# Performance work log

Hardware: AMD Instinct MI355X
Metric: run time of the kernel (lower is better)

Reference implementation:

```python
import jax, jax.numpy as jnp
import numpy as np

B, T, DIN, DOUT, H = 16, 4096, 64, 64, 128


def setup_inputs() -> dict:
    key = jax.random.key(0)
    ks = jax.random.split(key, 8)
    s_in = 1.0 / np.sqrt(DIN)       # ~ torch kaiming-uniform scale for Linear
    s_h = 0.5 / np.sqrt(2.0 * H)    # keep complex recurrence spectral radius ~0.5
    s_out = 1.0 / np.sqrt(H)
    return {
        "x_real": jax.random.normal(ks[0], (B, T, DIN), jnp.float32),
        "x_imag": jax.random.normal(ks[1], (B, T, DIN), jnp.float32),
        "Wi_real": jax.random.normal(ks[2], (H, DIN), jnp.float32) * s_in,
        "Wi_imag": jax.random.normal(ks[3], (H, DIN), jnp.float32) * s_in,
        "Wh_real": jax.random.normal(ks[4], (H, H), jnp.float32) * s_h,
        "Wh_imag": jax.random.normal(ks[5], (H, H), jnp.float32) * s_h,
        "Wo_real": jax.random.normal(ks[6], (DOUT, H), jnp.float32) * s_out,
        "Wo_imag": jax.random.normal(ks[7], (DOUT, H), jnp.float32) * s_out,
    }


def reference(x_real, x_imag, Wi_real, Wi_imag, Wh_real, Wh_imag, Wo_real, Wo_imag):
    # Recombine real/imag parts into complex64 (torch module uses complex Linear layers).
    x = x_real + 1j * x_imag                       # [B, T, DIN] complex64
    Wi = Wi_real + 1j * Wi_imag                    # [H, DIN]
    Wh = Wh_real + 1j * Wh_imag                    # [H, H]
    Wo = Wo_real + 1j * Wo_imag                    # [DOUT, H]

    # input_ff: torch Linear computes x @ W^T
    xp = jnp.einsum("btd,hd->bth", x, Wi)          # [B, T, H]

    WhT = Wh.T

    def step(h, xt):
        # h_{t+1} = x_proj_t + 1j * hidden_ff(h_t)
        h_next = xt + 1j * (h @ WhT)
        return h_next, h_next

    h0 = jnp.zeros((x.shape[0], Wh.shape[0]), dtype=xp.dtype)   # [B, H]
    _, hs = jax.lax.scan(step, h0, jnp.swapaxes(xp, 0, 1))      # hs: [T, B, H]
    hidden = jnp.swapaxes(hs, 0, 1)                             # [B, T, H]

    # output_ff
    out = jnp.einsum("bth,oh->bto", hidden, Wo)                 # [B, T, DOUT] complex64
    return out
```

## Files before the change

kernel.cpp:

```cpp
#include <hip/hip_runtime.h>
#include <stdint.h>

#define BB   16
#define TT   4096
#define DIN  64
#define DOUT 64
#define HH   128
#define LCH  64
#define WARM 32
#define SS   96
#define TAPS 32


typedef __attribute__((ext_vector_type(8))) short short8;
typedef __attribute__((ext_vector_type(4))) float f32x4;

__device__ __forceinline__ uint32_t f2bf(float f) {
  uint32_t x = __float_as_uint(f);
  return (x + 0x7FFFu + ((x >> 16) & 1u)) >> 16;
}
__device__ __forceinline__ uint32_t pack_bf(float re, float im) {
  return f2bf(re) | (f2bf(im) << 16);
}
__device__ __forceinline__ float bf_re(uint32_t u) { return __uint_as_float(u << 16); }
__device__ __forceinline__ float bf_im(uint32_t u) { return __uint_as_float(u & 0xFFFF0000u); }

__device__ __forceinline__ int fragIdx(int d, int o, int part, int kk) {
  const int ks = part * 2 + (kk >> 5);
  const int k32 = kk & 31;
  const int nt = o >> 4;
  const int lane = ((k32 >> 3) << 4) | (o & 15);
  return (((d * 16 + ks * 4 + nt) * 64) + lane) * 8 + (k32 & 7);
}

__device__ __forceinline__ void rot_i(int r, float re, float im,
                                      float& tr, float& ti) {
  switch (r & 3) {
    case 0: tr = re;  ti = im;  break;
    case 1: tr = -im; ti = re;  break;
    case 2: tr = -re; ti = -im; break;
    default: tr = im; ti = -re; break;
  }
}

__device__ __forceinline__ void matsq_dev(
    const float* __restrict__ ar, const float* __restrict__ ai,
    int fromPlanes, const float2* __restrict__ src, float2* __restrict__ dst,
    int tileId, unsigned char* smemraw) {
  float2* band  = (float2*)smemraw;
  float2* panel = (float2*)(smemraw + 16384);
  const int tid = threadIdx.x;
  const int ib = tileId >> 3, jb = tileId & 7;
  for (int idx = tid; idx < 16 * HH; idx += 512) {
    const int e = (ib * 16 + (idx >> 7)) * HH + (idx & 127);
    band[idx] = fromPlanes ? make_float2(ar[e], ai[e]) : src[e];
  }
  const int jt = tid & 15, it = (tid >> 4) & 15;
  float sre = 0.f, sim = 0.f;
  for (int kp = 0; kp < 4; ++kp) {
    __syncthreads();
    for (int idx = tid; idx < 32 * HH; idx += 512) {
      const int e = (kp * 32 + (idx >> 7)) * HH + (idx & 127);
      panel[idx] = fromPlanes ? make_float2(ar[e], ai[e]) : src[e];
    }
    __syncthreads();
    if (tid < 256) {
#pragma unroll 4
      for (int kk = 0; kk < 32; ++kk) {
        const float2 a = band[it * HH + kp * 32 + kk];
        const float2 bv = panel[kk * HH + jb * 16 + jt];
        sre = fmaf(a.x, bv.x, sre); sre = fmaf(-a.y, bv.y, sre);
        sim = fmaf(a.x, bv.y, sim); sim = fmaf(a.y, bv.x, sim);
      }
    }
  }
  if (tid < 256)
    dst[(ib * 16 + it) * HH + jb * 16 + jt] = make_float2(sre, sim);
}

__device__ __forceinline__ void pmul_dev(
    const float* __restrict__ ar, const float* __restrict__ ai, int aPlanes,
    const float2* __restrict__ Aflat,
    const float* __restrict__ sr, const float* __restrict__ si, int sPlanes,
    const float2* __restrict__ src,
    float2* __restrict__ dst, int tile, unsigned char* smemraw) {
  float2* Pl = (float2*)smemraw;
  const int tid = threadIdx.x;
  if (sPlanes) {
    for (int idx = tid; idx < 8192; idx += 512)
      Pl[idx] = make_float2(sr[idx], si[idx]);
  } else {
    const float4* s4 = (const float4*)src;
    float4* d4 = (float4*)Pl;
    for (int idx = tid; idx < 4096; idx += 512) d4[idx] = s4[idx];
  }
  __syncthreads();
  if (tid < 256) {
    const int i = tile * 16 + (tid >> 4);
    const int c0 = (tid & 15) * 4;
    float accr[4] = {0.f, 0.f, 0.f, 0.f}, acim[4] = {0.f, 0.f, 0.f, 0.f};
#pragma unroll 4
    for (int k = 0; k < 128; ++k) {
      const float2 a = aPlanes ? make_float2(ar[i * 128 + k], ai[i * 128 + k])
                               : Aflat[i * 128 + k];
      const float4 p01 = *(const float4*)&Pl[k * 64 + c0];
      const float4 p23 = *(const float4*)&Pl[k * 64 + c0 + 2];
      accr[0] = fmaf(a.x, p01.x, fmaf(-a.y, p01.y, accr[0]));
      acim[0] = fmaf(a.x, p01.y, fmaf(a.y, p01.x, acim[0]));
      accr[1] = fmaf(a.x, p01.z, fmaf(-a.y, p01.w, accr[1]));
      acim[1] = fmaf(a.x, p01.w, fmaf(a.y, p01.z, acim[1]));
      accr[2] = fmaf(a.x, p23.x, fmaf(-a.y, p23.y, accr[2]));
      acim[2] = fmaf(a.x, p23.y, fmaf(a.y, p23.x, acim[2]));
      accr[3] = fmaf(a.x, p23.z, fmaf(-a.y, p23.w, accr[3]));
      acim[3] = fmaf(a.x, p23.w, fmaf(a.y, p23.z, acim[3]));
    }
#pragma unroll
    for (int cc = 0; cc < 4; ++cc)
      dst[i * 64 + c0 + cc] = make_float2(accr[cc], acim[cc]);
  }
}

__global__ __launch_bounds__(512, 1) void k_s0(
    const float* __restrict__ wir, const float* __restrict__ wii,
    const float* __restrict__ whr, const float* __restrict__ whi,
    float2* __restrict__ ws) {
  __shared__ __align__(16) unsigned char smem[65536];
  float2* Wp0 = ws;
  float2* P   = ws + 32768;
  const int blk = blockIdx.x;
  if (blk < 64) {
    matsq_dev(whr, whi, 1, Wp0, Wp0, blk, smem);
  } else if (blk < 72) {
    pmul_dev(whr, whi, 1, Wp0, wir, wii, 1, Wp0, P + 8192, blk - 64, smem);
  } else {
    const int idx = (blk - 72) * 512 + threadIdx.x;
    P[idx] = make_float2(wir[idx], wii[idx]);
  }
}

__global__ __launch_bounds__(512, 1) void k_s1(
    const float* __restrict__ wir, const float* __restrict__ wii,
    float2* __restrict__ ws) {
  __shared__ __align__(16) unsigned char smem[65536];
  float2* Wp0 = ws;
  float2* Wp1 = ws + 16384;
  float2* P   = ws + 32768;
  const int blk = blockIdx.x;
  if (blk < 64) {
    matsq_dev(nullptr, nullptr, 0, Wp0, Wp1, blk, smem);
  } else if (blk < 72) {
    pmul_dev(nullptr, nullptr, 0, Wp0, wir, wii, 0, P,
             P + 16384, blk - 64, smem);
  } else {
    pmul_dev(nullptr, nullptr, 0, Wp0, wir, wii, 0, P + 8192,
             P + 24576, blk - 72, smem);
  }
}

__global__ __launch_bounds__(512, 1) void k_chain4(
    const float* __restrict__ wor, const float* __restrict__ woi,
    float2* __restrict__ ws) {
  __shared__ __align__(16) unsigned char smemraw[73472];
  const float2* P  = ws + 32768;
  const float2* M4 = ws + 16384;
  short* Wf = (short*)(ws + 65536);
  const int kk = (int)blockIdx.x >> 1;
  const int u  = (int)blockIdx.x & 1;
  float2* pb = (float2*)smemraw;
  float2* wo = (float2*)(smemraw + 4352);
  const int tid = threadIdx.x;
  const int mi = tid >> 2, mq = tid & 3;
  const int vo = tid >> 3, vg = tid & 7;

  float m4re[32], m4im[32];
  {
    const float4* g = (const float4*)(M4 + mi * 128 + mq * 32);
#pragma unroll
    for (int s = 0; s < 16; ++s) {
      const float4 v = g[s];
      m4re[2 * s] = v.x; m4im[2 * s] = v.y;
      m4re[2 * s + 1] = v.z; m4im[2 * s + 1] = v.w;
    }
  }
  for (int idx = tid; idx < 8192; idx += 512) {
    const int o = idx >> 7, h = idx & 127;
    wo[o * 135 + h + (h >> 4)] = make_float2(wor[o * 128 + h], woi[o * 128 + h]);
  }
  if (tid < 128) {
    pb[tid + (tid >> 4)]       = P[(size_t)u * 8192 + tid * 64 + kk];
    pb[272 + tid + (tid >> 4)] = P[(size_t)(u + 2) * 8192 + tid * 64 + kk];
  }
  __syncthreads();

  int cur = 0;
#pragma unroll 1
  for (int j = 0; j < 8; ++j) {
    const float2* qa = pb + cur * 136;
    const float2* qb = pb + 272 + cur * 136;
    float var = 0.f, vai = 0.f, vbr = 0.f, vbi = 0.f;
    {
      const float2* wrow = wo + vo * 135 + vg * 17;
      const float2* pra = qa + vg * 17;
      const float2* prb = qb + vg * 17;
#pragma unroll
      for (int s = 0; s < 16; ++s) {
        const float2 a = wrow[s];
        const float2 pa = pra[s];
        const float2 pv = prb[s];
        var = fmaf(a.x, pa.x, fmaf(-a.y, pa.y, var));
        vai = fmaf(a.x, pa.y, fmaf(a.y, pa.x, vai));
        vbr = fmaf(a.x, pv.x, fmaf(-a.y, pv.y, vbr));
        vbi = fmaf(a.x, pv.y, fmaf(a.y, pv.x, vbi));
      }
    }
    var += __shfl_xor(var, 1); vai += __shfl_xor(vai, 1);
    vbr += __shfl_xor(vbr, 1); vbi += __shfl_xor(vbi, 1);
    var += __shfl_xor(var, 2); vai += __shfl_xor(vai, 2);
    vbr += __shfl_xor(vbr, 2); vbi += __shfl_xor(vbi, 2);
    var += __shfl_xor(var, 4); vai += __shfl_xor(vai, 4);
    vbr += __shfl_xor(vbr, 4); vbi += __shfl_xor(vbi, 4);
    if (vg == 0) {
      float tr, ti;
      rot_i(u, var, vai, tr, ti);
      const int da = 4 * j + u;
      Wf[fragIdx(da, vo, 0, kk)] = (short)f2bf(tr);
      Wf[fragIdx(da, vo, 1, kk)] = (short)f2bf(-ti);
      rot_i(u + 2, vbr, vbi, tr, ti);
      const int db = 4 * j + u + 2;
      Wf[fragIdx(db, vo, 0, kk)] = (short)f2bf(tr);
      Wf[fragIdx(db, vo, 1, kk)] = (short)f2bf(-ti);
    }
    if (j < 7) {
      float nar = 0.f, nai = 0.f, nbr = 0.f, nbi = 0.f;
      const float2* pma = qa + mq * 34;
      const float2* pmb = qb + mq * 34;
#pragma unroll
      for (int s = 0; s < 32; ++s) {
        const float2 pa = pma[s + (s >> 4)];
        const float2 pv = pmb[s + (s >> 4)];
        nar = fmaf(m4re[s], pa.x, fmaf(-m4im[s], pa.y, nar));
        nai = fmaf(m4re[s], pa.y, fmaf(m4im[s], pa.x, nai));
        nbr = fmaf(m4re[s], pv.x, fmaf(-m4im[s], pv.y, nbr));
        nbi = fmaf(m4re[s], pv.y, fmaf(m4im[s], pv.x, nbi));
      }
      nar += __shfl_xor(nar, 1); nai += __shfl_xor(nai, 1);
      nbr += __shfl_xor(nbr, 1); nbi += __shfl_xor(nbi, 1);
      nar += __shfl_xor(nar, 2); nai += __shfl_xor(nai, 2);
      nbr += __shfl_xor(nbr, 2); nbi += __shfl_xor(nbi, 2);
      if (mq == 0) {
        pb[(cur ^ 1) * 136 + mi + (mi >> 4)] = make_float2(nar, nai);
        pb[272 + (cur ^ 1) * 136 + mi + (mi >> 4)] = make_float2(nbr, nbi);
      }
    }
    __syncthreads();
    cur ^= 1;
  }
}

__global__ __launch_bounds__(512, 1) void k_conv2(
    const float* __restrict__ xr, const float* __restrict__ xi,
    const short* __restrict__ Wf, float* __restrict__ out) {
  __shared__ __align__(16) unsigned char smem[73728];
  char* xs = (char*)smem;
  const int tid = threadIdx.x;
  const int b = blockIdx.x & 15;
  const int t0 = (blockIdx.x >> 4) * 256;

  for (int idx = tid; idx < 288 * 16; idx += 512) {
    const int r = idx >> 4;
    const int kq = (idx & 15) << 2;
    const int sw = (r & 7) << 4;
    const int t = t0 + r - 32;
    uint32_t r01 = 0u, r23 = 0u, i01 = 0u, i23 = 0u;
    if (t >= 0) {
      const size_t g = ((size_t)b * TT + t) * 64 + kq;
      const float4 vr = *(const float4*)(xr + g);
      const float4 vi = *(const float4*)(xi + g);
      r01 = f2bf(vr.x) | (f2bf(vr.y) << 16);
      r23 = f2bf(vr.z) | (f2bf(vr.w) << 16);
      i01 = f2bf(vi.x) | (f2bf(vi.y) << 16);
      i23 = f2bf(vi.z) | (f2bf(vi.w) << 16);
    }
    char* rowp = xs + r * 256;
    *(uint2*)(rowp + ((kq * 2) ^ sw))       = make_uint2(r01, r23);
    *(uint2*)(rowp + ((128 + kq * 2) ^ sw)) = make_uint2(i01, i23);
  }
  __syncthreads();

  const int w = tid >> 6;
  const int lane = tid & 63;
  const int wr = w >> 1;
  const int kh = w & 1;
  const int lm = lane & 15;
  const int kc8 = (lane >> 4) << 3;

  f32x4 acc[4][4];
#pragma unroll
  for (int mi = 0; mi < 4; ++mi)
#pragma unroll
    for (int nt = 0; nt < 4; ++nt) acc[mi][nt] = (f32x4){0.f, 0.f, 0.f, 0.f};

  short8 aqA[4], bqA[4], aqB[4], bqB[4];
#define FETCH(IT, AQ, BQ)                                                     \
  do {                                                                        \
    const int d_ = kh * 16 + ((IT) >> 2);                                     \
    const int ks_ = (IT) & 3;                                                 \
    const int rb_ = 32 - d_ + wr * 64 + lm;                                   \
    const int colb_ = ((ks_ >> 1) * 64 + (ks_ & 1) * 32 + kc8) * 2;           \
    _Pragma("unroll")                                                         \
    for (int nt_ = 0; nt_ < 4; ++nt_)                                         \
      BQ[nt_] = *(const short8*)(Wf +                                         \
          (((d_ * 16 + ks_ * 4 + nt_) * 64 + lane) << 3));                    \
    _Pragma("unroll")                                                         \
    for (int mi_ = 0; mi_ < 4; ++mi_) {                                       \
      const int r_ = rb_ + mi_ * 16;                                          \
      AQ[mi_] = *(const short8*)(xs + r_ * 256 +                              \
                                 (colb_ ^ ((r_ & 7) << 4)));                  \
    }                                                                         \
  } while (0)

#define MFMAGRP(AQ, BQ)                                                       \
  do {                                                                        \
    _Pragma("unroll")                                                         \
    for (int mi_ = 0; mi_ < 4; ++mi_)                                         \
      _Pragma("unroll")                                                       \
      for (int nt_ = 0; nt_ < 4; ++nt_)                                       \
        acc[mi_][nt_] = __builtin_amdgcn_mfma_f32_16x16x32_bf16(              \
            AQ[mi_], BQ[nt_], acc[mi_][nt_], 0, 0, 0);                        \
  } while (0)

  FETCH(0, aqA, bqA);
#pragma unroll 1
  for (int it = 0; it < 62; it += 2) {
    FETCH(it + 1, aqB, bqB);
    MFMAGRP(aqA, bqA);
    FETCH(it + 2, aqA, bqA);
    MFMAGRP(aqB, bqB);
  }
  FETCH(63, aqB, bqB);
  MFMAGRP(aqA, bqA);
  MFMAGRP(aqB, bqB);
#undef FETCH
#undef MFMAGRP

  __syncthreads();
  float* fred = (float*)smem;
  if (kh == 1) {
#pragma unroll
    for (int mi = 0; mi < 4; ++mi)
#pragma unroll
      for (int nt = 0; nt < 4; ++nt)
#pragma unroll
        for (int rg = 0; rg < 4; ++rg) {
          const int mloc = ((lane >> 4) << 2) + rg + mi * 16;
          fred[wr * 4160 + mloc * 65 + nt * 16 + lm] = acc[mi][nt][rg];
        }
  }
  __syncthreads();
  if (kh == 0) {
    const int mrow = wr * 64 + ((lane >> 4) << 2);
#pragma unroll
    for (int mi = 0; mi < 4; ++mi) {
#pragma unroll
      for (int nt = 0; nt < 4; ++nt) {
        const int o = nt * 16 + lm;
        float* p = out + ((size_t)b * TT + t0 + mrow + mi * 16) * 64 + o;
#pragma unroll
        for (int rg = 0; rg < 4; ++rg) {
          const int mloc = ((lane >> 4) << 2) + rg + mi * 16;
          p[(size_t)rg * 64] =
              acc[mi][nt][rg] + fred[wr * 4160 + mloc * 65 + o];
        }
      }
    }
  }
}

__global__ __launch_bounds__(256) void k_fused(
    const float* __restrict__ xr, const float* __restrict__ xi,
    const float* __restrict__ wir, const float* __restrict__ wii,
    const float* __restrict__ whr, const float* __restrict__ whi,
    const float* __restrict__ wor, const float* __restrict__ woi,
    float* __restrict__ out) {
  __shared__ __align__(16) unsigned char smem[63488];
  uint32_t* xpl  = (uint32_t*)smem;
  uint32_t* wiq  = (uint32_t*)(smem + 49152);
  uint32_t* xtq  = (uint32_t*)(smem + 57344);
  float2*   part = (float2*)(smem + 49152);
  float2*   hbuf = (float2*)(smem + 59392);
  uint32_t* woA  = (uint32_t*)smem;
  const int tid = threadIdx.x;
  const int c = blockIdx.x >> 4;
  const int b = blockIdx.x & 15;
  const int t0 = c * LCH - WARM;

  const int ho = tid & 31;
  const int tg = tid >> 5;
  float accr[4][12], acci[4][12];
#pragma unroll
  for (int a = 0; a < 4; ++a)
#pragma unroll
    for (int t = 0; t < 12; ++t) { accr[a][t] = 0.f; acci[a][t] = 0.f; }

#pragma unroll 1
  for (int q = 0; q < 4; ++q) {
    if (q) __syncthreads();
    for (int idx = tid; idx < 16 * HH; idx += 256) {
      const int dd = idx & 15, h = idx >> 4;
      const int g = h * DIN + q * 16 + dd;
      wiq[dd * 128 + h] = pack_bf(wir[g], wii[g]);
    }
    for (int idx = tid; idx < 16 * SS; idx += 256) {
      const int dd = idx & 15, s = idx >> 4;
      const int t = t0 + s;
      uint32_t v = 0u;
      if (t >= 0) {
        const size_t g = ((size_t)b * TT + t) * DIN + q * 16 + dd;
        v = pack_bf(xr[g], xi[g]);
      }
      xtq[dd * 96 + s] = v;
    }
    __syncthreads();
#pragma unroll 4
    for (int dd = 0; dd < 16; ++dd) {
      const uint4 wv  = *(const uint4*)&wiq[dd * 128 + ho * 4];
      const uint4 xv0 = *(const uint4*)&xtq[dd * 96 + tg * 12];
      const uint4 xv1 = *(const uint4*)&xtq[dd * 96 + tg * 12 + 4];
      const uint4 xv2 = *(const uint4*)&xtq[dd * 96 + tg * 12 + 8];
      float wre[4], wim[4], xre[12], xim[12];
      wre[0] = bf_re(wv.x); wim[0] = bf_im(wv.x);
      wre[1] = bf_re(wv.y); wim[1] = bf_im(wv.y);
      wre[2] = bf_re(wv.z); wim[2] = bf_im(wv.z);
      wre[3] = bf_re(wv.w); wim[3] = bf_im(wv.w);
      xre[0] = bf_re(xv0.x); xim[0] = bf_im(xv0.x);
      xre[1] = bf_re(xv0.y); xim[1] = bf_im(xv0.y);
      xre[2] = bf_re(xv0.z); xim[2] = bf_im(xv0.z);
      xre[3] = bf_re(xv0.w); xim[3] = bf_im(xv0.w);
      xre[4] = bf_re(xv1.x); xim[4] = bf_im(xv1.x);
      xre[5] = bf_re(xv1.y); xim[5] = bf_im(xv1.y);
      xre[6] = bf_re(xv1.z); xim[6] = bf_im(xv1.z);
      xre[7] = bf_re(xv1.w); xim[7] = bf_im(xv1.w);
      xre[8] = bf_re(xv2.x); xim[8] = bf_im(xv2.x);
      xre[9] = bf_re(xv2.y); xim[9] = bf_im(xv2.y);
      xre[10] = bf_re(xv2.z); xim[10] = bf_im(xv2.z);
      xre[11] = bf_re(xv2.w); xim[11] = bf_im(xv2.w);
#pragma unroll
      for (int a = 0; a < 4; ++a)
#pragma unroll
        for (int t = 0; t < 12; ++t) {
          accr[a][t] = fmaf(wre[a], xre[t], accr[a][t]);
          accr[a][t] = fmaf(-wim[a], xim[t], accr[a][t]);
          acci[a][t] = fmaf(wre[a], xim[t], acci[a][t]);
          acci[a][t] = fmaf(wim[a], xre[t], acci[a][t]);
        }
    }
  }
  __syncthreads();

#pragma unroll
  for (int tt = 0; tt < 12; ++tt) {
    uint4 v;
    v.x = pack_bf(accr[0][tt], acci[0][tt]);
    v.y = pack_bf(accr[1][tt], acci[1][tt]);
    v.z = pack_bf(accr[2][tt], acci[2][tt]);
    v.w = pack_bf(accr[3][tt], acci[3][tt]);
    *(uint4*)&xpl[(tg * 12 + tt) * 128 + ho * 4] = v;
  }
  if (tid < HH) hbuf[tid] = make_float2(0.f, 0.f);

  const int p8 = tid & 7;
  const int jg = tid >> 3;
  float wr[4][16], wim_[4][16];
#pragma unroll
  for (int a = 0; a < 4; ++a)
#pragma unroll
    for (int i = 0; i < 16; i += 4) {
      const float4 vr = *(const float4*)(whr + (size_t)(jg * 4 + a) * HH + p8 * 16 + i);
      wr[a][i] = vr.x; wr[a][i + 1] = vr.y; wr[a][i + 2] = vr.z; wr[a][i + 3] = vr.w;
      const float4 vi = *(const float4*)(whi + (size_t)(jg * 4 + a) * HH + p8 * 16 + i);
      wim_[a][i] = vi.x; wim_[a][i + 1] = vi.y; wim_[a][i + 2] = vi.z; wim_[a][i + 3] = vi.w;
    }
  __syncthreads();

#pragma unroll 1
  for (int s = 0; s < SS; ++s) {
    const uint32_t u = (tid < HH) ? xpl[s * 128 + tid] : 0u;
    float sre[4] = {0.f, 0.f, 0.f, 0.f}, sim[4] = {0.f, 0.f, 0.f, 0.f};
#pragma unroll
    for (int i = 0; i < 16; ++i) {
      const float2 hv = hbuf[i * 8 + p8];
#pragma unroll
      for (int a = 0; a < 4; ++a) {
        sre[a] = fmaf(wr[a][i], hv.x, sre[a]);
        sre[a] = fmaf(-wim_[a][i], hv.y, sre[a]);
        sim[a] = fmaf(wr[a][i], hv.y, sim[a]);
        sim[a] = fmaf(wim_[a][i], hv.x, sim[a]);
      }
    }
#pragma unroll
    for (int a = 0; a < 4; ++a)
      part[(jg * 4 + a) * 10 + p8] = make_float2(sre[a], sim[a]);
    __syncthreads();
    if (tid < HH) {
      const int j = tid;
      const float4 q0 = *(const float4*)&part[j * 10];
      const float4 q1 = *(const float4*)&part[j * 10 + 2];
      const float4 q2 = *(const float4*)&part[j * 10 + 4];
      const float4 q3 = *(const float4*)&part[j * 10 + 6];
      const float R = ((q0.x + q0.z) + (q1.x + q1.z)) + ((q2.x + q2.z) + (q3.x + q3.z));
      const float I = ((q0.y + q0.w) + (q1.y + q1.w)) + ((q2.y + q2.w) + (q3.y + q3.w));
      const float hr = bf_re(u) - I;
      const float hi = bf_im(u) + R;
      hbuf[(j & 15) * 8 + (j >> 4)] = make_float2(hr, hi);
      if (s >= WARM) xpl[s * 128 + j] = pack_bf(hr, hi);
    }
    __syncthreads();
  }

  const int og = tid & 15;
  const int tg2 = tid >> 4;
  float orr[4][4];
#pragma unroll
  for (int a = 0; a < 4; ++a)
#pragma unroll
    for (int t = 0; t < 4; ++t) orr[a][t] = 0.f;
#pragma unroll 1
  for (int kp = 0; kp < 2; ++kp) {
    __syncthreads();
    for (int idx = tid; idx < DOUT * 64; idx += 256) {
      const int o = idx >> 6, hh = idx & 63;
      woA[hh * 64 + o] = pack_bf(wor[(size_t)o * HH + kp * 64 + hh],
                                 woi[(size_t)o * HH + kp * 64 + hh]);
    }
    __syncthreads();
    for (int hh = 0; hh < 64; ++hh) {
      const uint4 wv = *(const uint4*)&woA[hh * 64 + og * 4];
      float wre[4], wimv[4];
      wre[0] = bf_re(wv.x); wimv[0] = bf_im(wv.x);
      wre[1] = bf_re(wv.y); wimv[1] = bf_im(wv.y);
      wre[2] = bf_re(wv.z); wimv[2] = bf_im(wv.z);
      wre[3] = bf_re(wv.w); wimv[3] = bf_im(wv.w);
#pragma unroll
      for (int tt = 0; tt < 4; ++tt) {
        const uint32_t hu = xpl[(WARM + tg2 * 4 + tt) * 128 + kp * 64 + hh];
        const float hre = bf_re(hu), him = bf_im(hu);
#pragma unroll
        for (int a = 0; a < 4; ++a) {
          orr[a][tt] = fmaf(wre[a], hre, orr[a][tt]);
          orr[a][tt] = fmaf(-wimv[a], him, orr[a][tt]);
        }
      }
    }
  }
#pragma unroll
  for (int tt = 0; tt < 4; ++tt) {
    float* po = out + ((size_t)b * TT + (size_t)c * LCH + tg2 * 4 + tt) * DOUT + og * 4;
    *(float4*)po = make_float4(orr[0][tt], orr[1][tt], orr[2][tt], orr[3][tt]);
  }
}

extern "C" void kernel_launch(void* const* d_in, const int* in_sizes, int n_in,
                              void* d_out, int out_size, void* d_ws, size_t ws_size,
                              hipStream_t stream) {
  const float* xr  = (const float*)d_in[0];
  const float* xi  = (const float*)d_in[1];
  const float* wir = (const float*)d_in[2];
  const float* wii = (const float*)d_in[3];
  const float* whr = (const float*)d_in[4];
  const float* whi = (const float*)d_in[5];
  const float* wor = (const float*)d_in[6];
  const float* woi = (const float*)d_in[7];
  float* out = (float*)d_out;
  (void)in_sizes; (void)n_in; (void)out_size;

  const size_t NEED = 1048576;
  if (ws_size >= NEED) {
    float2* ws = (float2*)d_ws;
    short* Wfr = (short*)(ws + 65536);
    k_s0<<<88, 512, 0, stream>>>(wir, wii, whr, whi, ws);
    k_s1<<<80, 512, 0, stream>>>(wir, wii, ws);
    k_chain4<<<128, 512, 0, stream>>>(wor, woi, ws);
    k_conv2<<<256, 512, 0, stream>>>(xr, xi, Wfr, out);
  } else {
    k_fused<<<(TT / LCH) * BB, 256, 0, stream>>>(
        xr, xi, wir, wii, whr, whi, wor, woi, out);
  }
}
```

Baseline: 161.5 us.

## Retile conv kernel to 64-step tiles with 4-way K split across waves

The conv kernel now uses 256-thread blocks, each handling 64 time steps instead of 256, launched as 1024 blocks instead of 256. Each of the four waves takes a quarter of the 32 taps, so the partial sums go through a two-stage tree reduction in shared memory. Shared memory per block falls to about 33KB and launch bounds allow four blocks per CU, which aims to fill the GPU better and raise occupancy. In exchange, the 32-row halo is reloaded for every 64-row tile instead of every 256, and extra syncs and shared-memory passes are needed for the reduction.

```diff
diff --git a/kernel.cpp b/kernel.cpp
--- a/kernel.cpp
+++ b/kernel.cpp
@@ -257,16 +257,16 @@
   }
 }
 
-__global__ __launch_bounds__(512, 1) void k_conv2(
+__global__ __launch_bounds__(256, 4) void k_conv2(
     const float* __restrict__ xr, const float* __restrict__ xi,
     const short* __restrict__ Wf, float* __restrict__ out) {
-  __shared__ __align__(16) unsigned char smem[73728];
+  __shared__ __align__(16) unsigned char smem[33280];
   char* xs = (char*)smem;
   const int tid = threadIdx.x;
   const int b = blockIdx.x & 15;
-  const int t0 = (blockIdx.x >> 4) * 256;
-
-  for (int idx = tid; idx < 288 * 16; idx += 512) {
+  const int t0 = (blockIdx.x >> 4) * 64;
+
+  for (int idx = tid; idx < 96 * 16; idx += 256) {
     const int r = idx >> 4;
     const int kq = (idx & 15) << 2;
     const int sw = (r & 7) << 4;
@@ -287,10 +287,8 @@
   }
   __syncthreads();
 
-  const int w = tid >> 6;
+  const int kh = tid >> 6;
   const int lane = tid & 63;
-  const int wr = w >> 1;
-  const int kh = w & 1;
   const int lm = lane & 15;
   const int kc8 = (lane >> 4) << 3;
 
@@ -303,9 +301,9 @@
   short8 aqA[4], bqA[4], aqB[4], bqB[4];
 #define FETCH(IT, AQ, BQ)                                                     \
   do {                                                                        \
-    const int d_ = kh * 16 + ((IT) >> 2);                                     \
+    const int d_ = kh * 8 + ((IT) >> 2);                                      \
     const int ks_ = (IT) & 3;                                                 \
-    const int rb_ = 32 - d_ + wr * 64 + lm;                                   \
+    const int rb_ = 32 - d_ + lm;                                             \
     const int colb_ = ((ks_ >> 1) * 64 + (ks_ & 1) * 32 + kc8) * 2;           \
     _Pragma("unroll")                                                         \
     for (int nt_ = 0; nt_ < 4; ++nt_)                                         \
@@ -331,34 +329,57 @@
 
   FETCH(0, aqA, bqA);
 #pragma unroll 1
-  for (int it = 0; it < 62; it += 2) {
+  for (int it = 0; it < 30; it += 2) {
     FETCH(it + 1, aqB, bqB);
     MFMAGRP(aqA, bqA);
     FETCH(it + 2, aqA, bqA);
     MFMAGRP(aqB, bqB);
   }
-  FETCH(63, aqB, bqB);
+  FETCH(31, aqB, bqB);
   MFMAGRP(aqA, bqA);
   MFMAGRP(aqB, bqB);
 #undef FETCH
 #undef MFMAGRP
 
   __syncthreads();
-  float* fred = (float*)smem;
-  if (kh == 1) {
+  float* fredA = (float*)smem;
+  float* fredB = (float*)(smem + 16640);
+  const int mbase = (lane >> 4) << 2;
+
+  if (kh == 1 || kh == 3) {
+    float* fr = (kh == 1) ? fredA : fredB;
 #pragma unroll
     for (int mi = 0; mi < 4; ++mi)
 #pragma unroll
       for (int nt = 0; nt < 4; ++nt)
 #pragma unroll
-        for (int rg = 0; rg < 4; ++rg) {
-          const int mloc = ((lane >> 4) << 2) + rg + mi * 16;
-          fred[wr * 4160 + mloc * 65 + nt * 16 + lm] = acc[mi][nt][rg];
-        }
+        for (int rg = 0; rg < 4; ++rg)
+          fr[(mbase + rg + mi * 16) * 65 + nt * 16 + lm] = acc[mi][nt][rg];
+  }
+  __syncthreads();
+  if (kh == 0 || kh == 2) {
+    const float* fr = (kh == 0) ? fredA : fredB;
+#pragma unroll
+    for (int mi = 0; mi < 4; ++mi)
+#pragma unroll
+      for (int nt = 0; nt < 4; ++nt)
+#pragma unroll
+        for (int rg = 0; rg < 4; ++rg)
+          acc[mi][nt][rg] += fr[(mbase + rg + mi * 16) * 65 + nt * 16 + lm];
+  }
+  __syncthreads();
+  if (kh == 2) {
+#pragma unroll
+    for (int mi = 0; mi < 4; ++mi)
+#pragma unroll
+      for (int nt = 0; nt < 4; ++nt)
+#pragma unroll
+        for (int rg = 0; rg < 4; ++rg)
+          fredA[(mbase + rg + mi * 16) * 65 + nt * 16 + lm] = acc[mi][nt][rg];
   }
   __syncthreads();
   if (kh == 0) {
-    const int mrow = wr * 64 + ((lane >> 4) << 2);
+    const int mrow = mbase;
 #pragma unroll
     for (int mi = 0; mi < 4; ++mi) {
 #pragma unroll
@@ -367,9 +388,8 @@
         float* p = out + ((size_t)b * TT + t0 + mrow + mi * 16) * 64 + o;
 #pragma unroll
         for (int rg = 0; rg < 4; ++rg) {
-          const int mloc = ((lane >> 4) << 2) + rg + mi * 16;
-          p[(size_t)rg * 64] =
-              acc[mi][nt][rg] + fred[wr * 4160 + mloc * 65 + o];
+          p[(size_t)rg * 64] = acc[mi][nt][rg] +
+              fredA[(mbase + rg + mi * 16) * 65 + o];
         }
       }
     }
@@ -580,7 +600,7 @@
     k_s0<<<88, 512, 0, stream>>>(wir, wii, whr, whi, ws);
     k_s1<<<80, 512, 0, stream>>>(wir, wii, ws);
     k_chain4<<<128, 512, 0, stream>>>(wor, woi, ws);
-    k_conv2<<<256, 512, 0, stream>>>(xr, xi, Wfr, out);
+    k_conv2<<<1024, 256, 0, stream>>>(xr, xi, Wfr, out);
   } else {
     k_fused<<<(TT / LCH) * BB, 256, 0, stream>>>(
         xr, xi, wir, wii, whr, whi, wor, woi, out);
```

New measurement: 159.6 us. Within noise of the previous version (-1.2%).
